# Performance work log

Measured on AMD Instinct MI355X. Metric: run time of the kernel, lower is better.

Reference implementation:

```python
import jax, jax.numpy as jnp
import numpy as np

C = 256; COUT = 256; G = 8; GC = C // G; K = 3; P = K * K
PAD = 1; DIL = 1; STR = 1
EPS = 1e-5


def _group_norm(x, gamma, beta, groups=32, eps=EPS):
    # x: (N,H,W,C), torch.nn.GroupNorm semantics (biased var)
    N, H, W, Cc = x.shape
    xg = x.reshape(N, H, W, groups, Cc // groups)
    mu = xg.mean(axis=(1, 2, 4), keepdims=True)
    var = xg.var(axis=(1, 2, 4), keepdims=True)
    xg = (xg - mu) * jax.lax.rsqrt(var + eps)
    return xg.reshape(N, H, W, Cc) * gamma + beta


def _conv2d(x, w, b, stride=1, pad=1, groups=1):
    y = jax.lax.conv_general_dilated(
        x, w, (stride, stride), [(pad, pad), (pad, pad)],
        dimension_numbers=('NHWC', 'HWIO', 'NHWC'),
        feature_group_count=groups)
    return y + b


def _bilinear_gather(img, px, py, Hin, Win):
    x0 = jnp.floor(px); y0 = jnp.floor(py)
    wx1 = px - x0; wy1 = py - y0
    out = jnp.zeros(img.shape[:1] + px.shape[1:] + img.shape[-1:], img.dtype)
    for xi, wx in ((x0, 1.0 - wx1), (x0 + 1.0, wx1)):
        for yi, wy in ((y0, 1.0 - wy1), (y0 + 1.0, wy1)):
            valid = (xi >= 0) & (xi < Win) & (yi >= 0) & (yi < Hin)
            idx = (jnp.clip(yi, 0, Hin - 1) * Win + jnp.clip(xi, 0, Win - 1)).astype(jnp.int32)
            vals = jnp.take_along_axis(img, idx[..., None], axis=1)
            out = out + vals * (wx * wy * valid)[..., None]
    return out


def _forward(x, w_in, b_in, dw_w, dw_b, ln_g, ln_b, w_off, b_off, w_mask, b_mask,
             w_out, b_out, gn1_g, gn1_b, conv1_w, conv1_b, gn2_g, gn2_b,
             down_w, down_b, gn3_g, gn3_b):
    xs = jnp.transpose(x, (0, 2, 3, 1))  # NHWC
    N, H, W, _ = xs.shape
    # ---- DCNv3 ----
    x_proj = xs @ w_in + b_in                              # input_proj
    t = _conv2d(xs, dw_w, dw_b, stride=STR, pad=(K - 1) // 2, groups=C)  # depthwise
    mu = t.mean(-1, keepdims=True)
    var = t.var(-1, keepdims=True)
    t = (t - mu) * jax.lax.rsqrt(var + EPS) * ln_g + ln_b  # LayerNorm
    t = jax.nn.gelu(t, approximate=False)
    offset = (t @ w_off + b_off).reshape(N, H, W, G, P, 2)  # (x,y) pairs
    mask = jax.nn.softmax((t @ w_mask + b_mask).reshape(N, H, W, G, P), axis=-1)

    Hin, Win = H + 2 * PAD, W + 2 * PAD
    xp = jnp.pad(x_proj, ((0, 0), (PAD, PAD), (PAD, PAD), (0, 0)))
    base = (DIL * (K - 1)) // 2 + 0.5
    ref_y = (base + jnp.arange(H, dtype=xs.dtype) * STR) / Hin
    ref_x = (base + jnp.arange(W, dtype=xs.dtype) * STR) / Win
    ry, rx = jnp.meshgrid(ref_y, ref_x, indexing='ij')
    ref = jnp.stack([rx, ry], -1)[None, :, :, None, None, :]  # (1,H,W,1,1,2)
    d = jnp.arange(K, dtype=xs.dtype) * DIL - (DIL * (K - 1)) // 2
    gx, gy = jnp.meshgrid(d, d, indexing='ij')  # x varies fastest over axis0 (torch order)
    grid = jnp.stack([gx / Win, gy / Hin], -1).reshape(P, 2)
    spatial = jnp.array([Win, Hin], xs.dtype)
    loc = ref + grid + offset / spatial          # normalized [0,1], offset_scale=1
    px = loc[..., 0] * Win - 0.5                 # align_corners=False pixel coords
    py = loc[..., 1] * Hin - 0.5

    L = H * W
    img = xp.reshape(N, Hin * Win, G, GC).transpose(0, 2, 1, 3).reshape(N * G, Hin * Win, GC)
    pxf = jnp.transpose(px, (0, 3, 1, 2, 4)).reshape(N * G, L * P)
    pyf = jnp.transpose(py, (0, 3, 1, 2, 4)).reshape(N * G, L * P)
    sampled = _bilinear_gather(img, pxf, pyf, Hin, Win).reshape(N, G, L, P, GC)
    m = jnp.transpose(mask, (0, 3, 1, 2, 4)).reshape(N, G, L, P)
    agg = jnp.einsum('nglpc,nglp->nglc', sampled, m)
    y = agg.transpose(0, 2, 1, 3).reshape(N, H, W, C)
    y = y @ w_out + b_out                        # output_proj
    # ---- block_out ----
    y = jax.nn.silu(_group_norm(y, gn1_g, gn1_b))
    y = _conv2d(y, conv1_w, conv1_b, stride=1, pad=1)
    y = jax.nn.silu(_group_norm(y, gn2_g, gn2_b))
    # ---- down_sample ----
    y = _conv2d(y, down_w, down_b, stride=2, pad=1)
    y = _group_norm(y, gn3_g, gn3_b)
    return jnp.transpose(y, (0, 3, 1, 2))  # back to NCHW


def setup_inputs() -> dict:
    key = jax.random.key(0)
    ks = jax.random.split(key, 10)
    f = jnp.float32
    nrm = lambda k, shape, s: jax.random.normal(k, shape, dtype=f) * s
    N, H, W = 4, 64, 64
    return {
        'x': jax.random.normal(ks[0], (N, C, H, W), dtype=f),
        'w_in': nrm(ks[1], (C, C), 0.05), 'b_in': jnp.zeros((C,), f),
        'dw_w': nrm(ks[2], (K, K, 1, C), 0.1), 'dw_b': jnp.zeros((C,), f),
        'ln_g': jnp.ones((C,), f), 'ln_b': jnp.zeros((C,), f),
        'w_off': nrm(ks[3], (C, 2 * G * P), 0.02), 'b_off': nrm(ks[4], (2 * G * P,), 1.0),
        'w_mask': nrm(ks[5], (C, G * P), 0.02), 'b_mask': jnp.zeros((G * P,), f),
        'w_out': nrm(ks[6], (C, C), 0.05), 'b_out': jnp.zeros((C,), f),
        'gn1_g': jnp.ones((C,), f), 'gn1_b': jnp.zeros((C,), f),
        'conv1_w': nrm(ks[7], (3, 3, C, C), 0.02), 'conv1_b': jnp.zeros((C,), f),
        'gn2_g': jnp.ones((C,), f), 'gn2_b': jnp.zeros((C,), f),
        'down_w': nrm(ks[8], (3, 3, C, COUT), 0.02), 'down_b': jnp.zeros((COUT,), f),
        'gn3_g': jnp.ones((COUT,), f), 'gn3_b': jnp.zeros((COUT,), f),
    }


def reference(x, w_in, b_in, dw_w, dw_b, ln_g, ln_b, w_off, b_off, w_mask, b_mask,
              w_out, b_out, gn1_g, gn1_b, conv1_w, conv1_b, gn2_g, gn2_b,
              down_w, down_b, gn3_g, gn3_b):
    return _forward(x, w_in, b_in, dw_w, dw_b, ln_g, ln_b, w_off, b_off, w_mask,
                    b_mask, w_out, b_out, gn1_g, gn1_b, conv1_w, conv1_b,
                    gn2_g, gn2_b, down_w, down_b, gn3_g, gn3_b)
```

## Files before the change

kernel.cpp:

```cpp
#include <hip/hip_runtime.h>
#include <hip/hip_bf16.h>
#include <math.h>


typedef __attribute__((ext_vector_type(8))) short bf16x8;
typedef __attribute__((ext_vector_type(4))) float f32x4;

__device__ __forceinline__ float blo(unsigned u){
  union { unsigned int i; float f; } v; v.i = u<<16; return v.f;
}
__device__ __forceinline__ float bhi(unsigned u){
  union { unsigned int i; float f; } v; v.i = u & 0xffff0000u; return v.f;
}
__device__ __forceinline__ unsigned short f2b(float f){
  __hip_bfloat16 h = __float2bfloat16(f);
  return *reinterpret_cast<unsigned short*>(&h);
}
__device__ __forceinline__ unsigned pk2(float lo, float hi){
  return (unsigned)f2b(lo) | ((unsigned)f2b(hi)<<16);
}

__device__ __forceinline__ void gload16(const void* g, void* l){
  auto gp = reinterpret_cast<const __attribute__((address_space(1))) uint32_t*>(
      reinterpret_cast<uintptr_t>(g));
  auto lp = reinterpret_cast<__attribute__((address_space(3))) uint32_t*>(
      reinterpret_cast<uintptr_t>(l));
  __builtin_amdgcn_global_load_lds(gp, lp, 16, 0, 0);
}

__global__ __launch_bounds__(256) void k_prep(
    const float* __restrict__ x,
    const float* __restrict__ w_in, const float* __restrict__ w_out,
    const float* __restrict__ conv1_w, const float* __restrict__ down_w,
    const float* __restrict__ w_off, const float* __restrict__ w_mask,
    const float* __restrict__ b_off, const float* __restrict__ b_mask,
    __hip_bfloat16* __restrict__ w_inT, __hip_bfloat16* __restrict__ w_outT,
    __hip_bfloat16* __restrict__ c1T, __hip_bfloat16* __restrict__ dnT,
    __hip_bfloat16* __restrict__ w_omT, float* __restrict__ bias_om,
    float* __restrict__ stats, __hip_bfloat16* __restrict__ R3,
    __hip_bfloat16* __restrict__ xs)
{
  int b = blockIdx.x;
  if (b < 160){
    __shared__ float tl[32][257];
    const float* W; __hip_bfloat16* WT; int Kd, kb;
    if (b < 8)      { W = w_in;    WT = w_inT;  Kd = 256;  kb = b; }
    else if (b <16) { W = w_out;   WT = w_outT; Kd = 256;  kb = b-8; }
    else if (b <88) { W = conv1_w; WT = c1T;    Kd = 2304; kb = b-16; }
    else            { W = down_w;  WT = dnT;    Kd = 2304; kb = b-88; }
    int k0 = kb*32;
    #pragma unroll
    for (int dk=0; dk<32; dk++) tl[dk][threadIdx.x] = W[(size_t)(k0+dk)*256 + threadIdx.x];
    __syncthreads();
    #pragma unroll
    for (int r=0; r<32; r++){
      int co = r*8 + (threadIdx.x>>5);
      int dk = threadIdx.x&31;
      WT[(size_t)co*Kd + k0 + dk] = __float2bfloat16(tl[dk][co]);
    }
  } else if (b < 416){
    int n = b - 160, k = threadIdx.x;
    float v = (n<144) ? w_off[(size_t)k*144 + n] : (n<216 ? w_mask[(size_t)k*72 + (n-144)] : 0.f);
    w_omT[(size_t)n*256 + k] = __float2bfloat16(v);
    if (k==0) bias_om[n] = (n<144) ? b_off[n] : (n<216 ? b_mask[n-144] : 0.f);
  } else if (b < 546){
    int gid = (b-416)*8 + (threadIdx.x>>5);
    if (gid >= 1040) return;
    int n = gid/260; int ci = gid - n*260;
    int r, c;
    if (ci < 66){ r = 0; c = ci; }
    else if (ci < 132){ r = 65; c = ci-66; }
    else { int q = ci-132; r = 1 + (q>>1); c = (q&1) ? 65 : 0; }
    uint4* p = (uint4*)(R3 + ((size_t)((n*66+r)*66+c))*256) + (threadIdx.x&31);
    *p = make_uint4(0,0,0,0);
  } else if (b == 546){
    stats[threadIdx.x] = 0.f;
    stats[256+threadIdx.x] = 0.f;
    stats[512+threadIdx.x] = 0.f;
  } else {
    __shared__ float tile[32][33];
    int t = b - 547;
    int n = t >> 10;
    int c0 = ((t >> 7) & 7) * 32;
    int hw0 = (t & 127) * 32;
    int tx = threadIdx.x & 31, ty = threadIdx.x >> 5;
    #pragma unroll
    for (int ii=0; ii<4; ii++){
      int ci = ty + ii*8;
      tile[ci][tx] = x[(size_t)(n*256 + c0+ci)*4096 + hw0 + tx];
    }
    __syncthreads();
    #pragma unroll
    for (int ii=0; ii<4; ii++){
      int hwi = ty + ii*8;
      xs[((size_t)n*4096 + hw0+hwi)*256 + c0 + tx] = __float2bfloat16(tile[tx][hwi]);
    }
  }
}

template<int AMODE, int OMODE, int STRIDE, int KTOT, int NSHIFT>
__global__ __launch_bounds__(256) void k_mm(
    const __hip_bfloat16* __restrict__ A, const __hip_bfloat16* __restrict__ Bt,
    const float* __restrict__ bias, float* __restrict__ OF, __hip_bfloat16* __restrict__ OH,
    float* __restrict__ stats)
{
  constexpr int AROWS = 64;
  constexpr int MI = AROWS/32;
  constexpr int WROWS = AROWS/2;
  constexpr int JA = AROWS*128/4096;
  constexpr int BUFSZ = AROWS*128 + 16384;
  __shared__ uint4 lds4[3*BUFSZ/16];
  char* ldsc = (char*)lds4;
  const int tid = threadIdx.x;
  const int lane = tid & 63;
  const int wv = tid >> 6;
  const int wr = wv >> 1, wc = wv & 1;

  int id = blockIdx.y * gridDim.x + blockIdx.x;
  int cpx = (gridDim.x * gridDim.y) >> 3;
  int sw = (id & 7) * cpx + (id >> 3);
  const int m0 = (sw >> 1) * AROWS, n0 = (sw & 1) * 128;

  const int swz_s = ((tid >> 3) & 7) << 4;
  const int cby = ((tid & 7) << 4) ^ swz_s;
  const int kl = cby >> 1;
  int aoff[JA], boff[4];
  #pragma unroll
  for (int j=0;j<JA;j++){
    int row = j*32 + (tid>>3);
    if (AMODE==0){
      aoff[j] = (m0 + row) * KTOT + kl;
    } else {
      int m = m0 + row;
      int n, ho, wo;
      if (STRIDE==1){ n = m>>12; ho = (m>>6)&63; wo = m&63; }
      else          { n = m>>10; ho = (m>>5)&31; wo = m&31; }
      aoff[j] = ((n*66 + ho*STRIDE)*66 + wo*STRIDE)*256 + kl;
    }
  }
  #pragma unroll
  for (int j=0;j<4;j++) boff[j] = (n0 + j*32 + (tid>>3)) * KTOT + kl;
  char* ldsst = ldsc + wv*1024;

  const int fr = lane & 15;
  const int kb = (lane >> 4) << 4;
  const int swz_r = (fr & 7) << 4;
  int aRow[MI], bRow[4];
  #pragma unroll
  for (int i=0;i<MI;i++) aRow[i] = (wr*WROWS + i*16 + fr) * 128;
  #pragma unroll
  for (int i=0;i<4;i++)  bRow[i] = AROWS*128 + (wc*64 + i*16 + fr) * 128;
  int cb[2];
  cb[0] = kb ^ swz_r;
  cb[1] = (64 | kb) ^ swz_r;

  float bn[4];
  #pragma unroll
  for (int ni=0;ni<4;ni++) bn[ni] = bias[n0 + wc*64 + ni*16 + fr];

  f32x4 acc[MI][4];
  #pragma unroll
  for (int mi=0;mi<MI;mi++)
    #pragma unroll
    for (int ni=0;ni<4;ni++)
      acc[mi][ni] = (f32x4){0.f,0.f,0.f,0.f};

  auto STAGE = [&](int buf, int t){
    const int k0 = t*64;
    int astep;
    if (AMODE==1){
      int tap = k0 >> 8;
      int kh = (tap>=6) ? 2 : (tap>=3 ? 1 : 0);
      int kw = tap - kh*3;
      astep = (kh*66 + kw)*256 + (k0 & 255);
    } else astep = k0;
    char* db = ldsst + buf*BUFSZ;
    #pragma unroll
    for (int j=0;j<JA;j++) gload16(A + aoff[j] + astep, db + j*4096);
    #pragma unroll
    for (int j=0;j<4;j++)  gload16(Bt + boff[j] + k0, db + AROWS*128 + j*4096);
  };

  constexpr int NT = KTOT / 64;
  STAGE(0, 0);
  STAGE(1, 1);
  asm volatile("s_waitcnt vmcnt(6)" ::: "memory");
  __builtin_amdgcn_s_barrier();
  __builtin_amdgcn_sched_barrier(0);
  for (int t=0; t<NT; ++t){
    if (t+2 < NT) STAGE((t+2)%3, t+2);
    char* cbase = ldsc + (t%3)*BUFSZ;
    __builtin_amdgcn_s_setprio(1);
    #pragma unroll
    for (int kk=0; kk<2; kk++){
      bf16x8 av[MI], bv[4];
      #pragma unroll
      for (int i=0;i<MI;i++) av[i] = *(const bf16x8*)(cbase + aRow[i] + cb[kk]);
      #pragma unroll
      for (int i=0;i<4;i++)  bv[i] = *(const bf16x8*)(cbase + bRow[i] + cb[kk]);
      #pragma unroll
      for (int mi=0;mi<MI;mi++)
        #pragma unroll
        for (int ni=0;ni<4;ni++)
          acc[mi][ni] = __builtin_amdgcn_mfma_f32_16x16x32_bf16(av[mi], bv[ni], acc[mi][ni], 0,0,0);
    }
    __builtin_amdgcn_s_setprio(0);
    if (t < NT-1){
      if (t+2 < NT) asm volatile("s_waitcnt vmcnt(6)" ::: "memory");
      else          asm volatile("s_waitcnt vmcnt(0)" ::: "memory");
      __builtin_amdgcn_s_barrier();
      __builtin_amdgcn_sched_barrier(0);
    }
  }

  float sni[4] = {0.f,0.f,0.f,0.f};
  float qni[4] = {0.f,0.f,0.f,0.f};
  #pragma unroll
  for (int mi=0;mi<MI;mi++){
    #pragma unroll
    for (int r=0;r<4;r++){
      int gr = m0 + wr*WROWS + mi*16 + (lane>>4)*4 + r;
      #pragma unroll
      for (int ni=0;ni<4;ni++){
        int gc = n0 + wc*64 + ni*16 + fr;
        float v = acc[mi][ni][r] + bn[ni];
        if (NSHIFT){ sni[ni] += v; qni[ni] += v*v; }
        if (OMODE==0){
          OH[(size_t)gr*256 + gc] = __float2bfloat16(v);
        } else if (OMODE==1){
          int n = gr>>12, h = (gr>>6)&63, w = gr&63;
          OH[((size_t)((n*66)+(h+1))*66 + (w+1))*256 + gc] = __float2bfloat16(v);
        } else {
          if (gc < 216) OF[(size_t)gr*216 + gc] = v;
        }
      }
    }
  }
  if (NSHIFT){
    #pragma unroll
    for (int ni=0;ni<4;ni++){
      #pragma unroll
      for (int msk=16; msk<64; msk<<=1){
        sni[ni] += __shfl_xor(sni[ni], msk);
        qni[ni] += __shfl_xor(qni[ni], msk);
      }
      #pragma unroll
      for (int msk=1; msk<8; msk<<=1){
        sni[ni] += __shfl_xor(sni[ni], msk);
        qni[ni] += __shfl_xor(qni[ni], msk);
      }
    }
    __syncthreads();
    float* ls = (float*)ldsc;
    if (tid < 32) ls[tid] = 0.f;
    __syncthreads();
    if ((lane & 7) == 0 && (lane & 48) == 0){
      int oct = (lane>>3) & 1;
      #pragma unroll
      for (int ni=0;ni<4;ni++){
        int idx = wc*8 + ni*2 + oct;
        atomicAdd(&ls[idx], sni[ni]);
        atomicAdd(&ls[16+idx], qni[ni]);
      }
    }
    __syncthreads();
    if (tid < 16){
      int gg = (m0>>NSHIFT)*32 + (n0>>3) + tid;
      atomicAdd(&stats[gg*2+0], ls[tid]);
      atomicAdd(&stats[gg*2+1], ls[16+tid]);
    }
  }
}

__global__ __launch_bounds__(256) void k_dwln(
    const __hip_bfloat16* __restrict__ xs, const float* __restrict__ dw_w, const float* __restrict__ dw_b,
    const float* __restrict__ ln_g, const float* __restrict__ ln_b, __hip_bfloat16* __restrict__ t)
{
  __shared__ float lw[9*256];
  __shared__ float lb[256], lg[256], lbt[256];
  int tid = threadIdx.x;
  #pragma unroll
  for (int p=0;p<9;p++) lw[p*256+tid] = dw_w[p*256+tid];
  lb[tid] = dw_b[tid]; lg[tid] = ln_g[tid]; lbt[tid] = ln_b[tid];
  __syncthreads();
  int posl = tid>>5, cg = tid&31, c0 = cg*8;
  int pos = blockIdx.x*8 + posl;
  int nb = pos>>12, h = (pos>>6)&63, w = pos&63;
  float v[8];
  #pragma unroll
  for (int k=0;k<8;k++) v[k] = lb[c0+k];
  #pragma unroll
  for (int kh=0;kh<3;kh++){
    int hin = h+kh-1;
    if (hin<0||hin>=64) continue;
    #pragma unroll
    for (int kw=0;kw<3;kw++){
      int win = w+kw-1;
      if (win<0||win>=64) continue;
      const unsigned short* xr = (const unsigned short*)xs + ((size_t)((nb*64+hin)*64+win))*256 + c0;
      uint4 u = *(const uint4*)xr;
      const float* wr = &lw[(kh*3+kw)*256 + c0];
      v[0] += blo(u.x)*wr[0]; v[1] += bhi(u.x)*wr[1];
      v[2] += blo(u.y)*wr[2]; v[3] += bhi(u.y)*wr[3];
      v[4] += blo(u.z)*wr[4]; v[5] += bhi(u.z)*wr[5];
      v[6] += blo(u.w)*wr[6]; v[7] += bhi(u.w)*wr[7];
    }
  }
  float s=0.f, s2=0.f;
  #pragma unroll
  for (int k=0;k<8;k++){ s += v[k]; s2 += v[k]*v[k]; }
  #pragma unroll
  for (int m=1;m<32;m<<=1){ s += __shfl_xor(s,m); s2 += __shfl_xor(s2,m); }
  float mu = s*(1.f/256.f);
  float var = s2*(1.f/256.f) - mu*mu;
  float rstd = rsqrtf(var + 1e-5f);
  float ge[8];
  #pragma unroll
  for (int k=0;k<8;k++){
    float xn = (v[k]-mu)*rstd*lg[c0+k] + lbt[c0+k];
    ge[k] = 0.5f*xn*(1.f + erff(xn*0.70710678118654752f));
  }
  uint4 o;
  o.x = pk2(ge[0],ge[1]); o.y = pk2(ge[2],ge[3]);
  o.z = pk2(ge[4],ge[5]); o.w = pk2(ge[6],ge[7]);
  *(uint4*)((unsigned short*)t + (size_t)pos*256 + c0) = o;
}

__global__ __launch_bounds__(256) void k_sample(
    const __hip_bfloat16* __restrict__ xp, const float* __restrict__ D, __hip_bfloat16* __restrict__ y)
{
  int tid = threadIdx.x;
  int pp = tid>>5;
  int g = (tid>>2)&7, li = tid&3;
  int pos = blockIdx.x*8 + pp;
  int nb = pos >> 12, h = (pos >> 6) & 63, w = pos & 63;
  const float* Dp = D + (size_t)pos*216;
  const float* offp = Dp + g*18;
  const float* mskp = Dp + 144 + g*9;
  float mr[9];
  #pragma unroll
  for (int p=0;p<9;p++) mr[p] = mskp[p];
  float mx = mr[0];
  #pragma unroll
  for (int p=1;p<9;p++) mx = fmaxf(mx, mr[p]);
  float ssum = 0.f;
  #pragma unroll
  for (int p=0;p<9;p++){ mr[p] = __expf(mr[p]-mx); ssum += mr[p]; }
  float rinv = 1.f/ssum;
  const unsigned short* img = (const unsigned short*)xp + (size_t)nb*4356*256 + g*32 + li*8;
  float a0=0,a1=0,a2=0,a3=0,a4=0,a5=0,a6=0,a7=0;
  #pragma unroll
  for (int p=0;p<9;p++){
    int di = p/3 - 1, dj = p%3 - 1;
    float2 off = *(const float2*)(offp + p*2);
    float px = (float)(w + 1 + di) + off.x;
    float py = (float)(h + 1 + dj) + off.y;
    float x0f = floorf(px), y0f = floorf(py);
    float wx1 = px - x0f, wy1 = py - y0f;
    float wx0 = 1.f - wx1, wy0 = 1.f - wy1;
    int x0 = (int)x0f, y0 = (int)y0f;
    float s0=0,s1=0,s2=0,s3=0,s4=0,s5=0,s6=0,s7=0;
    #pragma unroll
    for (int cy=0;cy<2;cy++){
      int yi = y0+cy;
      if (yi<0||yi>=66) continue;
      float wy = cy ? wy1 : wy0;
      #pragma unroll
      for (int cx=0;cx<2;cx++){
        int xi = x0+cx;
        if (xi<0||xi>=66) continue;
        float wq = (cx ? wx1 : wx0)*wy;
        uint4 u = *(const uint4*)(img + (size_t)(yi*66+xi)*256);
        s0 += blo(u.x)*wq; s1 += bhi(u.x)*wq;
        s2 += blo(u.y)*wq; s3 += bhi(u.y)*wq;
        s4 += blo(u.z)*wq; s5 += bhi(u.z)*wq;
        s6 += blo(u.w)*wq; s7 += bhi(u.w)*wq;
      }
    }
    float mp = mr[p]*rinv;
    a0 += s0*mp; a1 += s1*mp; a2 += s2*mp; a3 += s3*mp;
    a4 += s4*mp; a5 += s5*mp; a6 += s6*mp; a7 += s7*mp;
  }
  uint4 o;
  o.x = pk2(a0,a1); o.y = pk2(a2,a3); o.z = pk2(a4,a5); o.w = pk2(a6,a7);
  *(uint4*)((unsigned short*)y + (size_t)pos*256 + g*32 + li*8) = o;
}

__global__ __launch_bounds__(256) void k_gnapply(
    const __hip_bfloat16* __restrict__ X, const float* __restrict__ stats,
    const float* __restrict__ gamma, const float* __restrict__ beta,
    __hip_bfloat16* __restrict__ OH, int nmain)
{
  int b = blockIdx.x;
  int tid = threadIdx.x;
  if (b >= nmain){
    int gid = (b - nmain)*8 + (tid>>5);
    if (gid >= 1040) return;
    int n = gid/260; int ci = gid - n*260;
    int r, c;
    if (ci < 66){ r = 0; c = ci; }
    else if (ci < 132){ r = 65; c = ci-66; }
    else { int q = ci-132; r = 1 + (q>>1); c = (q&1) ? 65 : 0; }
    uint4* p = (uint4*)(OH + ((size_t)((n*66+r)*66+c))*256) + (tid&31);
    *p = make_uint4(0,0,0,0);
    return;
  }
  int row = b*8 + (tid>>5);
  int grp = tid & 31;
  int c0 = grp*8;
  int nb = row >> 12;
  float S  = stats[(nb*32+grp)*2+0];
  float S2 = stats[(nb*32+grp)*2+1];
  const float inv = 1.f/32768.f;
  float mu = S*inv;
  float rs = rsqrtf(S2*inv - mu*mu + 1e-5f);
  float4 g0 = *(const float4*)(gamma + c0), g1 = *(const float4*)(gamma + c0 + 4);
  float4 bt0 = *(const float4*)(beta + c0), bt1 = *(const float4*)(beta + c0 + 4);
  uint4 u = *(const uint4*)((const unsigned short*)X + (size_t)row*256 + c0);
  float v[8] = { blo(u.x), bhi(u.x), blo(u.y), bhi(u.y), blo(u.z), bhi(u.z), blo(u.w), bhi(u.w) };
  float gm[8] = { g0.x,g0.y,g0.z,g0.w,g1.x,g1.y,g1.z,g1.w };
  float bb[8] = { bt0.x,bt0.y,bt0.z,bt0.w,bt1.x,bt1.y,bt1.z,bt1.w };
  #pragma unroll
  for (int k=0;k<8;k++){
    float t = (v[k]-mu)*rs*gm[k] + bb[k];
    v[k] = t / (1.f + expf(-t));
  }
  int h = (row>>6)&63, w = row&63;
  uint4 o;
  o.x = pk2(v[0],v[1]); o.y = pk2(v[2],v[3]); o.z = pk2(v[4],v[5]); o.w = pk2(v[6],v[7]);
  *(uint4*)((unsigned short*)OH + ((size_t)((nb*66)+(h+1))*66 + (w+1))*256 + c0) = o;
}

__global__ __launch_bounds__(256) void k_gnout(
    const __hip_bfloat16* __restrict__ X, const float* __restrict__ stats,
    const float* __restrict__ gamma, const float* __restrict__ beta, float* __restrict__ out)
{
  __shared__ float val[8][1024];
  int nb = blockIdx.x >> 5, cg = blockIdx.x & 31;
  int c0 = cg*8;
  float S  = stats[(nb*32+cg)*2+0];
  float S2 = stats[(nb*32+cg)*2+1];
  const float inv = 1.f/8192.f;
  float mu = S*inv;
  float rs = rsqrtf(S2*inv - mu*mu + 1e-5f);
  float4 g0 = *(const float4*)(gamma + c0), g1 = *(const float4*)(gamma + c0 + 4);
  float4 bt0 = *(const float4*)(beta + c0), bt1 = *(const float4*)(beta + c0 + 4);
  float gm[8] = { g0.x,g0.y,g0.z,g0.w,g1.x,g1.y,g1.z,g1.w };
  float bb[8] = { bt0.x,bt0.y,bt0.z,bt0.w,bt1.x,bt1.y,bt1.z,bt1.w };
  #pragma unroll
  for (int k=0;k<4;k++){
    int pos = k*256 + threadIdx.x;
    uint4 u = *(const uint4*)((const unsigned short*)X + ((size_t)(nb*1024+pos))*256 + c0);
    float v[8] = { blo(u.x), bhi(u.x), blo(u.y), bhi(u.y), blo(u.z), bhi(u.z), blo(u.w), bhi(u.w) };
    #pragma unroll
    for (int q=0;q<8;q++) val[q][pos] = (v[q]-mu)*rs*gm[q] + bb[q];
  }
  __syncthreads();
  int ch = threadIdx.x>>5, pl = threadIdx.x&31;
  float* orow = out + (((size_t)(nb*256 + c0 + ch))<<10);
  #pragma unroll
  for (int j=0;j<32;j++) orow[pl + j*32] = val[ch][pl + j*32];
}

extern "C" void kernel_launch(void* const* d_in, const int* in_sizes, int n_in,
                              void* d_out, int out_size, void* d_ws, size_t ws_size,
                              hipStream_t stream) {
  const float* x      = (const float*)d_in[0];
  const float* w_in   = (const float*)d_in[1];
  const float* b_in   = (const float*)d_in[2];
  const float* dw_w   = (const float*)d_in[3];
  const float* dw_b   = (const float*)d_in[4];
  const float* ln_g   = (const float*)d_in[5];
  const float* ln_b   = (const float*)d_in[6];
  const float* w_off  = (const float*)d_in[7];
  const float* b_off  = (const float*)d_in[8];
  const float* w_mask = (const float*)d_in[9];
  const float* b_mask = (const float*)d_in[10];
  const float* w_out  = (const float*)d_in[11];
  const float* b_out  = (const float*)d_in[12];
  const float* gn1_g  = (const float*)d_in[13];
  const float* gn1_b  = (const float*)d_in[14];
  const float* conv1_w= (const float*)d_in[15];
  const float* conv1_b= (const float*)d_in[16];
  const float* gn2_g  = (const float*)d_in[17];
  const float* gn2_b  = (const float*)d_in[18];
  const float* down_w = (const float*)d_in[19];
  const float* down_b = (const float*)d_in[20];
  const float* gn3_g  = (const float*)d_in[21];
  const float* gn3_b  = (const float*)d_in[22];
  float* out = (float*)d_out;

  char* wsb = (char*)d_ws;
  __hip_bfloat16* R0h = (__hip_bfloat16*)wsb;
  float* R1f = (float*)(wsb + 16777216);
  __hip_bfloat16* R1h = (__hip_bfloat16*)(wsb + 16777216);
  __hip_bfloat16* R2 = (__hip_bfloat16*)(wsb + 33554432);
  __hip_bfloat16* R3 = (__hip_bfloat16*)(wsb + 41943040);
  __hip_bfloat16* R4 = (__hip_bfloat16*)(wsb + 50864128);
  char* R5 = wsb + 59785216;
  __hip_bfloat16* w_inT  = (__hip_bfloat16*)R5;
  __hip_bfloat16* w_outT = (__hip_bfloat16*)(R5 + 131072);
  __hip_bfloat16* w_omT  = (__hip_bfloat16*)(R5 + 262144);
  __hip_bfloat16* c1T    = (__hip_bfloat16*)(R5 + 393216);
  __hip_bfloat16* dnT    = (__hip_bfloat16*)(R5 + 1572864);
  float* bias_om         = (float*)(R5 + 2752512);
  float* stats           = (float*)(R5 + 2753536);

  k_prep<<<4643, 256, 0, stream>>>(x, w_in, w_out, conv1_w, down_w, w_off, w_mask, b_off, b_mask,
                                   w_inT, w_outT, c1T, dnT, w_omT, bias_om, stats, R3, R2);
  k_mm<0,1,1,256,0><<<dim3(256,2), 256, 0, stream>>>(R2, w_inT, b_in, nullptr, R3, nullptr);
  k_dwln<<<2048, 256, 0, stream>>>(R2, dw_w, dw_b, ln_g, ln_b, R4);
  k_mm<0,2,1,256,0><<<dim3(256,2), 256, 0, stream>>>(R4, w_omT, bias_om, R1f, nullptr, nullptr);
  k_sample<<<2048, 256, 0, stream>>>(R3, R1f, R2);
  k_mm<0,0,1,256,12><<<dim3(256,2), 256, 0, stream>>>(R2, w_outT, b_out, nullptr, R0h, stats);
  k_gnapply<<<2048+130, 256, 0, stream>>>(R0h, stats, gn1_g, gn1_b, R4, 2048);
  k_mm<1,0,1,2304,12><<<dim3(256,2), 256, 0, stream>>>(R4, c1T, conv1_b, nullptr, R1h, stats+256);
  k_gnapply<<<2048+130, 256, 0, stream>>>(R1h, stats+256, gn2_g, gn2_b, R3, 2048);
  k_mm<1,0,2,2304,10><<<dim3(64,2), 256, 0, stream>>>(R3, dnT, down_b, nullptr, R0h, stats+512);
  k_gnout<<<128, 256, 0, stream>>>(R0h, stats+512, gn3_g, gn3_b, out);
}
```

Before: 235.3 us.

## Fuse all stages into one persistent kernel with atomic grid barriers

Replaces the eleven separate launches with a single persistent kernel of 512 blocks that runs every stage in turn, separated by atomic-counter grid barriers. Elementwise stages are remapped so each block processes rows it produced in the preceding GEMM tile, and the final strided conv switches to 32-row tiles over 256 blocks. The goal is to remove launch gaps and tail effects between kernels and to improve cache locality. In exchange the kernel depends on all 512 blocks being co-resident (two per CU), spends time in spin barriers, and leaves blocks idle during the smaller stages.

```diff
diff --git a/kernel.cpp b/kernel.cpp
--- a/kernel.cpp
+++ b/kernel.cpp
@@ -3,6 +3,8 @@
 #include <math.h>
 
 
+#define NBLK 512
+
 typedef __attribute__((ext_vector_type(8))) short bf16x8;
 typedef __attribute__((ext_vector_type(4))) float f32x4;
 
@@ -21,14 +23,26 @@
 }
 
 __device__ __forceinline__ void gload16(const void* g, void* l){
-  auto gp = reinterpret_cast<const __attribute__((address_space(1))) uint32_t*>(
+  auto gp = reinterpret_cast<const __attribute__((address_space(1))) unsigned*>(
       reinterpret_cast<uintptr_t>(g));
-  auto lp = reinterpret_cast<__attribute__((address_space(3))) uint32_t*>(
+  auto lp = reinterpret_cast<__attribute__((address_space(3))) unsigned*>(
       reinterpret_cast<uintptr_t>(l));
   __builtin_amdgcn_global_load_lds(gp, lp, 16, 0, 0);
 }
 
-__global__ __launch_bounds__(256) void k_prep(
+__device__ __forceinline__ void gridsync(unsigned* c){
+  __syncthreads();
+  if (threadIdx.x == 0){
+    __threadfence();
+    atomicAdd(c, 1u);
+    while (__hip_atomic_load(c, __ATOMIC_RELAXED, __HIP_MEMORY_SCOPE_AGENT) < (unsigned)NBLK)
+      __builtin_amdgcn_s_sleep(1);
+    __threadfence();
+  }
+  __syncthreads();
+}
+
+__device__ void prep_unit(int b, char* smem,
     const float* __restrict__ x,
     const float* __restrict__ w_in, const float* __restrict__ w_out,
     const float* __restrict__ conv1_w, const float* __restrict__ down_w,
@@ -40,9 +54,9 @@
     float* __restrict__ stats, __hip_bfloat16* __restrict__ R3,
     __hip_bfloat16* __restrict__ xs)
 {
-  int b = blockIdx.x;
+  __syncthreads();
   if (b < 160){
-    __shared__ float tl[32][257];
+    float (*tl)[257] = (float(*)[257])smem;
     const float* W; __hip_bfloat16* WT; int Kd, kb;
     if (b < 8)      { W = w_in;    WT = w_inT;  Kd = 256;  kb = b; }
     else if (b <16) { W = w_out;   WT = w_outT; Kd = 256;  kb = b-8; }
@@ -78,7 +92,7 @@
     stats[256+threadIdx.x] = 0.f;
     stats[512+threadIdx.x] = 0.f;
   } else {
-    __shared__ float tile[32][33];
+    float (*tile)[33] = (float(*)[33])smem;
     int t = b - 547;
     int n = t >> 10;
     int c0 = ((t >> 7) & 7) * 32;
@@ -98,27 +112,25 @@
   }
 }
 
-template<int AMODE, int OMODE, int STRIDE, int KTOT, int NSHIFT>
-__global__ __launch_bounds__(256) void k_mm(
+#define WAITV(n) asm volatile("s_waitcnt vmcnt(" #n ")" ::: "memory")
+
+template<int AMODE, int OMODE, int STRIDE, int KTOT, int NSHIFT, int AROWS, int NWG>
+__device__ void mm_body(int id,
     const __hip_bfloat16* __restrict__ A, const __hip_bfloat16* __restrict__ Bt,
     const float* __restrict__ bias, float* __restrict__ OF, __hip_bfloat16* __restrict__ OH,
-    float* __restrict__ stats)
+    float* __restrict__ stats, char* ldsc)
 {
-  constexpr int AROWS = 64;
   constexpr int MI = AROWS/32;
   constexpr int WROWS = AROWS/2;
-  constexpr int JA = AROWS*128/4096;
+  constexpr int JA = AROWS/32;
+  constexpr int SL = JA + 4;
   constexpr int BUFSZ = AROWS*128 + 16384;
-  __shared__ uint4 lds4[3*BUFSZ/16];
-  char* ldsc = (char*)lds4;
   const int tid = threadIdx.x;
   const int lane = tid & 63;
   const int wv = tid >> 6;
   const int wr = wv >> 1, wc = wv & 1;
 
-  int id = blockIdx.y * gridDim.x + blockIdx.x;
-  int cpx = (gridDim.x * gridDim.y) >> 3;
-  int sw = (id & 7) * cpx + (id >> 3);
+  int sw = (id & 7) * (NWG >> 3) + (id >> 3);
   const int m0 = (sw >> 1) * AROWS, n0 = (sw & 1) * 128;
 
   const int swz_s = ((tid >> 3) & 7) << 4;
@@ -184,7 +196,7 @@
   constexpr int NT = KTOT / 64;
   STAGE(0, 0);
   STAGE(1, 1);
-  asm volatile("s_waitcnt vmcnt(6)" ::: "memory");
+  if constexpr (SL==6) WAITV(6); else WAITV(5);
   __builtin_amdgcn_s_barrier();
   __builtin_amdgcn_sched_barrier(0);
   for (int t=0; t<NT; ++t){
@@ -206,8 +218,8 @@
     }
     __builtin_amdgcn_s_setprio(0);
     if (t < NT-1){
-      if (t+2 < NT) asm volatile("s_waitcnt vmcnt(6)" ::: "memory");
-      else          asm volatile("s_waitcnt vmcnt(0)" ::: "memory");
+      if (t+2 < NT){ if constexpr (SL==6) WAITV(6); else WAITV(5); }
+      else WAITV(0);
       __builtin_amdgcn_s_barrier();
       __builtin_amdgcn_sched_barrier(0);
     }
@@ -272,19 +284,13 @@
   }
 }
 
-__global__ __launch_bounds__(256) void k_dwln(
-    const __hip_bfloat16* __restrict__ xs, const float* __restrict__ dw_w, const float* __restrict__ dw_b,
-    const float* __restrict__ ln_g, const float* __restrict__ ln_b, __hip_bfloat16* __restrict__ t)
+__device__ void dwln_unit(int l, const __hip_bfloat16* __restrict__ xs,
+    const float* lw, const float* lb, const float* lg, const float* lbt,
+    __hip_bfloat16* __restrict__ t)
 {
-  __shared__ float lw[9*256];
-  __shared__ float lb[256], lg[256], lbt[256];
   int tid = threadIdx.x;
-  #pragma unroll
-  for (int p=0;p<9;p++) lw[p*256+tid] = dw_w[p*256+tid];
-  lb[tid] = dw_b[tid]; lg[tid] = ln_g[tid]; lbt[tid] = ln_b[tid];
-  __syncthreads();
   int posl = tid>>5, cg = tid&31, c0 = cg*8;
-  int pos = blockIdx.x*8 + posl;
+  int pos = l*8 + posl;
   int nb = pos>>12, h = (pos>>6)&63, w = pos&63;
   float v[8];
   #pragma unroll
@@ -326,17 +332,16 @@
   *(uint4*)((unsigned short*)t + (size_t)pos*256 + c0) = o;
 }
 
-__global__ __launch_bounds__(256) void k_sample(
-    const __hip_bfloat16* __restrict__ xp, const float* __restrict__ D, __hip_bfloat16* __restrict__ y)
+__device__ void sample_unit(int l, const float* Ds,
+    const __hip_bfloat16* __restrict__ xp, __hip_bfloat16* __restrict__ y)
 {
   int tid = threadIdx.x;
   int pp = tid>>5;
   int g = (tid>>2)&7, li = tid&3;
-  int pos = blockIdx.x*8 + pp;
+  int pos = l*8 + pp;
   int nb = pos >> 12, h = (pos >> 6) & 63, w = pos & 63;
-  const float* Dp = D + (size_t)pos*216;
-  const float* offp = Dp + g*18;
-  const float* mskp = Dp + 144 + g*9;
+  const float* offp = Ds + pp*216 + g*18;
+  const float* mskp = Ds + pp*216 + 144 + g*9;
   float mr[9];
   #pragma unroll
   for (int p=0;p<9;p++) mr[p] = mskp[p];
@@ -352,9 +357,9 @@
   #pragma unroll
   for (int p=0;p<9;p++){
     int di = p/3 - 1, dj = p%3 - 1;
-    float2 off = *(const float2*)(offp + p*2);
-    float px = (float)(w + 1 + di) + off.x;
-    float py = (float)(h + 1 + dj) + off.y;
+    float ox = offp[p*2], oy = offp[p*2+1];
+    float px = (float)(w + 1 + di) + ox;
+    float py = (float)(h + 1 + dj) + oy;
     float x0f = floorf(px), y0f = floorf(py);
     float wx1 = px - x0f, wy1 = py - y0f;
     float wx0 = 1.f - wx1, wy0 = 1.f - wy1;
@@ -386,26 +391,12 @@
   *(uint4*)((unsigned short*)y + (size_t)pos*256 + g*32 + li*8) = o;
 }
 
-__global__ __launch_bounds__(256) void k_gnapply(
-    const __hip_bfloat16* __restrict__ X, const float* __restrict__ stats,
-    const float* __restrict__ gamma, const float* __restrict__ beta,
-    __hip_bfloat16* __restrict__ OH, int nmain)
+__device__ void gnap_main(int u, const __hip_bfloat16* __restrict__ X,
+    const float* __restrict__ stats, const float* __restrict__ gamma,
+    const float* __restrict__ beta, __hip_bfloat16* __restrict__ OH)
 {
-  int b = blockIdx.x;
   int tid = threadIdx.x;
-  if (b >= nmain){
-    int gid = (b - nmain)*8 + (tid>>5);
-    if (gid >= 1040) return;
-    int n = gid/260; int ci = gid - n*260;
-    int r, c;
-    if (ci < 66){ r = 0; c = ci; }
-    else if (ci < 132){ r = 65; c = ci-66; }
-    else { int q = ci-132; r = 1 + (q>>1); c = (q&1) ? 65 : 0; }
-    uint4* p = (uint4*)(OH + ((size_t)((n*66+r)*66+c))*256) + (tid&31);
-    *p = make_uint4(0,0,0,0);
-    return;
-  }
-  int row = b*8 + (tid>>5);
+  int row = u*8 + (tid>>5);
   int grp = tid & 31;
   int c0 = grp*8;
   int nb = row >> 12;
@@ -416,8 +407,8 @@
   float rs = rsqrtf(S2*inv - mu*mu + 1e-5f);
   float4 g0 = *(const float4*)(gamma + c0), g1 = *(const float4*)(gamma + c0 + 4);
   float4 bt0 = *(const float4*)(beta + c0), bt1 = *(const float4*)(beta + c0 + 4);
-  uint4 u = *(const uint4*)((const unsigned short*)X + (size_t)row*256 + c0);
-  float v[8] = { blo(u.x), bhi(u.x), blo(u.y), bhi(u.y), blo(u.z), bhi(u.z), blo(u.w), bhi(u.w) };
+  uint4 u4 = *(const uint4*)((const unsigned short*)X + (size_t)row*256 + c0);
+  float v[8] = { blo(u4.x), bhi(u4.x), blo(u4.y), bhi(u4.y), blo(u4.z), bhi(u4.z), blo(u4.w), bhi(u4.w) };
   float gm[8] = { g0.x,g0.y,g0.z,g0.w,g1.x,g1.y,g1.z,g1.w };
   float bb[8] = { bt0.x,bt0.y,bt0.z,bt0.w,bt1.x,bt1.y,bt1.z,bt1.w };
   #pragma unroll
@@ -431,12 +422,24 @@
   *(uint4*)((unsigned short*)OH + ((size_t)((nb*66)+(h+1))*66 + (w+1))*256 + c0) = o;
 }
 
-__global__ __launch_bounds__(256) void k_gnout(
-    const __hip_bfloat16* __restrict__ X, const float* __restrict__ stats,
-    const float* __restrict__ gamma, const float* __restrict__ beta, float* __restrict__ out)
+__device__ void gnap_border(int u, __hip_bfloat16* __restrict__ OH){
+  int gid = u*8 + (threadIdx.x>>5);
+  if (gid >= 1040) return;
+  int n = gid/260; int ci = gid - n*260;
+  int r, c;
+  if (ci < 66){ r = 0; c = ci; }
+  else if (ci < 132){ r = 65; c = ci-66; }
+  else { int q = ci-132; r = 1 + (q>>1); c = (q&1) ? 65 : 0; }
+  uint4* p = (uint4*)(OH + ((size_t)((n*66+r)*66+c))*256) + (threadIdx.x&31);
+  *p = make_uint4(0,0,0,0);
+}
+
+__device__ void gnout_unit(int u, const __hip_bfloat16* __restrict__ X,
+    const float* __restrict__ stats, const float* __restrict__ gamma,
+    const float* __restrict__ beta, float* __restrict__ out, char* smem)
 {
-  __shared__ float val[8][1024];
-  int nb = blockIdx.x >> 5, cg = blockIdx.x & 31;
+  float (*val)[1024] = (float(*)[1024])smem;
+  int nb = u >> 5, cg = u & 31;
   int c0 = cg*8;
   float S  = stats[(nb*32+cg)*2+0];
   float S2 = stats[(nb*32+cg)*2+1];
@@ -450,8 +453,8 @@
   #pragma unroll
   for (int k=0;k<4;k++){
     int pos = k*256 + threadIdx.x;
-    uint4 u = *(const uint4*)((const unsigned short*)X + ((size_t)(nb*1024+pos))*256 + c0);
-    float v[8] = { blo(u.x), bhi(u.x), blo(u.y), bhi(u.y), blo(u.z), bhi(u.z), blo(u.w), bhi(u.w) };
+    uint4 u4 = *(const uint4*)((const unsigned short*)X + ((size_t)(nb*1024+pos))*256 + c0);
+    float v[8] = { blo(u4.x), bhi(u4.x), blo(u4.y), bhi(u4.y), blo(u4.z), bhi(u4.z), blo(u4.w), bhi(u4.w) };
     #pragma unroll
     for (int q=0;q<8;q++) val[q][pos] = (v[q]-mu)*rs*gm[q] + bb[q];
   }
@@ -460,6 +463,102 @@
   float* orow = out + (((size_t)(nb*256 + c0 + ch))<<10);
   #pragma unroll
   for (int j=0;j<32;j++) orow[pl + j*32] = val[ch][pl + j*32];
+}
+
+__global__ __launch_bounds__(256, 2) void k_mega(
+    const float* __restrict__ x,
+    const float* __restrict__ w_in, const float* __restrict__ b_in,
+    const float* __restrict__ dw_w, const float* __restrict__ dw_b,
+    const float* __restrict__ ln_g, const float* __restrict__ ln_b,
+    const float* __restrict__ w_off, const float* __restrict__ b_off,
+    const float* __restrict__ w_mask, const float* __restrict__ b_mask,
+    const float* __restrict__ w_out, const float* __restrict__ b_out,
+    const float* __restrict__ gn1_g, const float* __restrict__ gn1_b,
+    const float* __restrict__ conv1_w, const float* __restrict__ conv1_b,
+    const float* __restrict__ gn2_g, const float* __restrict__ gn2_b,
+    const float* __restrict__ down_w, const float* __restrict__ down_b,
+    const float* __restrict__ gn3_g, const float* __restrict__ gn3_b,
+    float* __restrict__ out,
+    __hip_bfloat16* R0h, float* R1f, __hip_bfloat16* R2,
+    __hip_bfloat16* R3, __hip_bfloat16* R4,
+    __hip_bfloat16* w_inT, __hip_bfloat16* w_outT, __hip_bfloat16* w_omT,
+    __hip_bfloat16* c1T, __hip_bfloat16* dnT,
+    float* bias_om, float* stats, unsigned* sync)
+{
+  __shared__ __align__(16) char SMEM[73728];
+  __hip_bfloat16* R1h = (__hip_bfloat16*)R1f;
+  const int bid = blockIdx.x;
+  const int s8 = bid>>3, x8 = bid&7;
+
+  for (int b = bid; b < 4643; b += NBLK)
+    prep_unit(b, SMEM, x, w_in, w_out, conv1_w, down_w, w_off, w_mask, b_off, b_mask,
+              w_inT, w_outT, c1T, dnT, w_omT, bias_om, stats, R3, R2);
+  gridsync(sync+0);
+
+  mm_body<0,1,1,256,0,64,NBLK>(bid, R2, w_inT, b_in, nullptr, R3, nullptr, SMEM);
+  __syncthreads();
+  {
+    float* lw = (float*)SMEM;
+    float* lb = (float*)(SMEM+9216);
+    float* lg = (float*)(SMEM+10240);
+    float* lbt= (float*)(SMEM+11264);
+    int tid = threadIdx.x;
+    #pragma unroll
+    for (int p=0;p<9;p++) lw[p*256+tid] = dw_w[p*256+tid];
+    lb[tid] = dw_b[tid]; lg[tid] = ln_g[tid]; lbt[tid] = ln_b[tid];
+    __syncthreads();
+    #pragma unroll
+    for (int j=0;j<4;j++){
+      int l = (x8>>1)*512 + (s8*2+(x8&1))*4 + j;
+      dwln_unit(l, R2, lw, lb, lg, lbt, R4);
+    }
+  }
+  gridsync(sync+1);
+
+  mm_body<0,2,1,256,0,64,NBLK>(bid, R4, w_omT, bias_om, R1f, nullptr, nullptr, SMEM);
+  gridsync(sync+2);
+
+  #pragma unroll
+  for (int j=0;j<4;j++){
+    int l = (x8>>1)*512 + (s8*2+(x8&1))*4 + j;
+    __syncthreads();
+    float4* dst = (float4*)SMEM;
+    const float4* src = (const float4*)(R1f + (size_t)l*8*216);
+    int tid = threadIdx.x;
+    if (tid < 216){ dst[tid] = src[tid]; dst[tid+216] = src[tid+216]; }
+    __syncthreads();
+    sample_unit(l, (const float*)SMEM, R3, R2);
+  }
+  gridsync(sync+3);
+
+  mm_body<0,0,1,256,12,64,NBLK>(bid, R2, w_outT, b_out, nullptr, R0h, stats, SMEM);
+  gridsync(sync+4);
+
+  #pragma unroll
+  for (int j=0;j<4;j++){
+    int u = (x8>>1)*512 + (s8*2+(x8&1))*4 + j;
+    gnap_main(u, R0h, stats, gn1_g, gn1_b, R4);
+  }
+  for (int u = bid; u < 130; u += NBLK) gnap_border(u, R4);
+  gridsync(sync+5);
+
+  mm_body<1,0,1,2304,12,64,NBLK>(bid, R4, c1T, conv1_b, nullptr, R1h, stats+256, SMEM);
+  gridsync(sync+6);
+
+  #pragma unroll
+  for (int j=0;j<4;j++){
+    int u = (x8>>1)*512 + (s8*2+(x8&1))*4 + j;
+    gnap_main(u, R1h, stats+256, gn2_g, gn2_b, R3);
+  }
+  for (int u = bid; u < 130; u += NBLK) gnap_border(u, R3);
+  gridsync(sync+7);
+
+  if (bid < 256)
+    mm_body<1,0,2,2304,10,32,256>(bid, R3, dnT, down_b, nullptr, R0h, stats+512, SMEM);
+  gridsync(sync+8);
+
+  if (bid < 128)
+    gnout_unit(bid, R0h, stats+512, gn3_g, gn3_b, out, SMEM);
 }
 
 extern "C" void kernel_launch(void* const* d_in, const int* in_sizes, int n_in,
@@ -493,7 +592,6 @@
   char* wsb = (char*)d_ws;
   __hip_bfloat16* R0h = (__hip_bfloat16*)wsb;
   float* R1f = (float*)(wsb + 16777216);
-  __hip_bfloat16* R1h = (__hip_bfloat16*)(wsb + 16777216);
   __hip_bfloat16* R2 = (__hip_bfloat16*)(wsb + 33554432);
   __hip_bfloat16* R3 = (__hip_bfloat16*)(wsb + 41943040);
   __hip_bfloat16* R4 = (__hip_bfloat16*)(wsb + 50864128);
@@ -505,17 +603,13 @@
   __hip_bfloat16* dnT    = (__hip_bfloat16*)(R5 + 1572864);
   float* bias_om         = (float*)(R5 + 2752512);
   float* stats           = (float*)(R5 + 2753536);
-
-  k_prep<<<4643, 256, 0, stream>>>(x, w_in, w_out, conv1_w, down_w, w_off, w_mask, b_off, b_mask,
-                                   w_inT, w_outT, c1T, dnT, w_omT, bias_om, stats, R3, R2);
-  k_mm<0,1,1,256,0><<<dim3(256,2), 256, 0, stream>>>(R2, w_inT, b_in, nullptr, R3, nullptr);
-  k_dwln<<<2048, 256, 0, stream>>>(R2, dw_w, dw_b, ln_g, ln_b, R4);
-  k_mm<0,2,1,256,0><<<dim3(256,2), 256, 0, stream>>>(R4, w_omT, bias_om, R1f, nullptr, nullptr);
-  k_sample<<<2048, 256, 0, stream>>>(R3, R1f, R2);
-  k_mm<0,0,1,256,12><<<dim3(256,2), 256, 0, stream>>>(R2, w_outT, b_out, nullptr, R0h, stats);
-  k_gnapply<<<2048+130, 256, 0, stream>>>(R0h, stats, gn1_g, gn1_b, R4, 2048);
-  k_mm<1,0,1,2304,12><<<dim3(256,2), 256, 0, stream>>>(R4, c1T, conv1_b, nullptr, R1h, stats+256);
-  k_gnapply<<<2048+130, 256, 0, stream>>>(R1h, stats+256, gn2_g, gn2_b, R3, 2048);
-  k_mm<1,0,2,2304,10><<<dim3(64,2), 256, 0, stream>>>(R3, dnT, down_b, nullptr, R0h, stats+512);
-  k_gnout<<<128, 256, 0, stream>>>(R0h, stats+512, gn3_g, gn3_b, out);
-}
+  unsigned* syncc        = (unsigned*)(R5 + 2756608);
+
+  hipMemsetAsync(syncc, 0, 64, stream);
+  k_mega<<<NBLK, 256, 0, stream>>>(
+      x, w_in, b_in, dw_w, dw_b, ln_g, ln_b, w_off, b_off, w_mask, b_mask,
+      w_out, b_out, gn1_g, gn1_b, conv1_w, conv1_b, gn2_g, gn2_b,
+      down_w, down_b, gn3_g, gn3_b, out,
+      R0h, R1f, R2, R3, R4, w_inT, w_outT, w_omT, c1T, dnT,
+      bias_om, stats, syncc);
+}
```

New measurement: 672.9 us. 186% more time.

## Merge input-projection GEMM and depthwise-LN into one launch; stage sampler params in LDS

Applied to the files above, without the earlier changes.

The input_proj GEMM and the depthwise conv + LayerNorm + GELU kernel both read only xs, so they now run as one launch: the first 512 blocks do the GEMM and the remaining 2048 do the depthwise work. This removes a launch boundary and lets the two independent jobs overlap on the GPU. The sampler kernel now copies each block's offset/mask rows from global memory into shared memory with coalesced float4 loads before use. The price is that the dwln blocks now reserve the GEMM's full 72KB of LDS, which may cut their occupancy.

```diff
diff --git a/kernel.cpp b/kernel.cpp
--- a/kernel.cpp
+++ b/kernel.cpp
@@ -21,12 +21,14 @@
 }
 
 __device__ __forceinline__ void gload16(const void* g, void* l){
-  auto gp = reinterpret_cast<const __attribute__((address_space(1))) uint32_t*>(
+  auto gp = reinterpret_cast<const __attribute__((address_space(1))) unsigned*>(
       reinterpret_cast<uintptr_t>(g));
-  auto lp = reinterpret_cast<__attribute__((address_space(3))) uint32_t*>(
+  auto lp = reinterpret_cast<__attribute__((address_space(3))) unsigned*>(
       reinterpret_cast<uintptr_t>(l));
   __builtin_amdgcn_global_load_lds(gp, lp, 16, 0, 0);
 }
+
+#define WAITV(n) asm volatile("s_waitcnt vmcnt(" #n ")" ::: "memory")
 
 __global__ __launch_bounds__(256) void k_prep(
     const float* __restrict__ x,
@@ -98,27 +100,23 @@
   }
 }
 
-template<int AMODE, int OMODE, int STRIDE, int KTOT, int NSHIFT>
-__global__ __launch_bounds__(256) void k_mm(
+template<int AMODE, int OMODE, int STRIDE, int KTOT, int NSHIFT, int NWG>
+__device__ __forceinline__ void mm_body(int id,
     const __hip_bfloat16* __restrict__ A, const __hip_bfloat16* __restrict__ Bt,
     const float* __restrict__ bias, float* __restrict__ OF, __hip_bfloat16* __restrict__ OH,
-    float* __restrict__ stats)
+    float* __restrict__ stats, char* ldsc)
 {
   constexpr int AROWS = 64;
-  constexpr int MI = AROWS/32;
-  constexpr int WROWS = AROWS/2;
-  constexpr int JA = AROWS*128/4096;
+  constexpr int MI = 2;
+  constexpr int WROWS = 32;
+  constexpr int JA = 2;
   constexpr int BUFSZ = AROWS*128 + 16384;
-  __shared__ uint4 lds4[3*BUFSZ/16];
-  char* ldsc = (char*)lds4;
   const int tid = threadIdx.x;
   const int lane = tid & 63;
   const int wv = tid >> 6;
   const int wr = wv >> 1, wc = wv & 1;
 
-  int id = blockIdx.y * gridDim.x + blockIdx.x;
-  int cpx = (gridDim.x * gridDim.y) >> 3;
-  int sw = (id & 7) * cpx + (id >> 3);
+  int sw = (id & 7) * (NWG >> 3) + (id >> 3);
   const int m0 = (sw >> 1) * AROWS, n0 = (sw & 1) * 128;
 
   const int swz_s = ((tid >> 3) & 7) << 4;
@@ -184,7 +182,7 @@
   constexpr int NT = KTOT / 64;
   STAGE(0, 0);
   STAGE(1, 1);
-  asm volatile("s_waitcnt vmcnt(6)" ::: "memory");
+  WAITV(6);
   __builtin_amdgcn_s_barrier();
   __builtin_amdgcn_sched_barrier(0);
   for (int t=0; t<NT; ++t){
@@ -206,8 +204,8 @@
     }
     __builtin_amdgcn_s_setprio(0);
     if (t < NT-1){
-      if (t+2 < NT) asm volatile("s_waitcnt vmcnt(6)" ::: "memory");
-      else          asm volatile("s_waitcnt vmcnt(0)" ::: "memory");
+      if (t+2 < NT){ WAITV(6); }
+      else WAITV(0);
       __builtin_amdgcn_s_barrier();
       __builtin_amdgcn_sched_barrier(0);
     }
@@ -272,19 +270,24 @@
   }
 }
 
-__global__ __launch_bounds__(256) void k_dwln(
-    const __hip_bfloat16* __restrict__ xs, const float* __restrict__ dw_w, const float* __restrict__ dw_b,
-    const float* __restrict__ ln_g, const float* __restrict__ ln_b, __hip_bfloat16* __restrict__ t)
-{
-  __shared__ float lw[9*256];
-  __shared__ float lb[256], lg[256], lbt[256];
+template<int AMODE, int OMODE, int STRIDE, int KTOT, int NSHIFT, int NWG>
+__global__ __launch_bounds__(256) void k_mm(
+    const __hip_bfloat16* __restrict__ A, const __hip_bfloat16* __restrict__ Bt,
+    const float* __restrict__ bias, float* __restrict__ OF, __hip_bfloat16* __restrict__ OH,
+    float* __restrict__ stats)
+{
+  __shared__ __align__(16) char SMEM[73728];
+  int id = blockIdx.y * gridDim.x + blockIdx.x;
+  mm_body<AMODE,OMODE,STRIDE,KTOT,NSHIFT,NWG>(id, A, Bt, bias, OF, OH, stats, SMEM);
+}
+
+__device__ __forceinline__ void dwln_unit(int l, const __hip_bfloat16* __restrict__ xs,
+    const float* lw, const float* lb, const float* lg, const float* lbt,
+    __hip_bfloat16* __restrict__ t)
+{
   int tid = threadIdx.x;
-  #pragma unroll
-  for (int p=0;p<9;p++) lw[p*256+tid] = dw_w[p*256+tid];
-  lb[tid] = dw_b[tid]; lg[tid] = ln_g[tid]; lbt[tid] = ln_b[tid];
-  __syncthreads();
   int posl = tid>>5, cg = tid&31, c0 = cg*8;
-  int pos = blockIdx.x*8 + posl;
+  int pos = l*8 + posl;
   int nb = pos>>12, h = (pos>>6)&63, w = pos&63;
   float v[8];
   #pragma unroll
@@ -326,17 +329,48 @@
   *(uint4*)((unsigned short*)t + (size_t)pos*256 + c0) = o;
 }
 
+__global__ __launch_bounds__(256) void k_p1(
+    const __hip_bfloat16* __restrict__ xs, const __hip_bfloat16* __restrict__ w_inT,
+    const float* __restrict__ b_in, __hip_bfloat16* __restrict__ R3,
+    const float* __restrict__ dw_w, const float* __restrict__ dw_b,
+    const float* __restrict__ ln_g, const float* __restrict__ ln_b,
+    __hip_bfloat16* __restrict__ t)
+{
+  __shared__ __align__(16) char SMEM[73728];
+  int bid = blockIdx.x;
+  if (bid < 512){
+    mm_body<0,1,1,256,0,512>(bid, xs, w_inT, b_in, nullptr, R3, nullptr, SMEM);
+  } else {
+    float* lw = (float*)SMEM;
+    float* lb = (float*)(SMEM+9216);
+    float* lg = (float*)(SMEM+10240);
+    float* lbt= (float*)(SMEM+11264);
+    int tid = threadIdx.x;
+    #pragma unroll
+    for (int p=0;p<9;p++) lw[p*256+tid] = dw_w[p*256+tid];
+    lb[tid] = dw_b[tid]; lg[tid] = ln_g[tid]; lbt[tid] = ln_b[tid];
+    __syncthreads();
+    dwln_unit(bid-512, xs, lw, lb, lg, lbt, t);
+  }
+}
+
 __global__ __launch_bounds__(256) void k_sample(
     const __hip_bfloat16* __restrict__ xp, const float* __restrict__ D, __hip_bfloat16* __restrict__ y)
 {
+  __shared__ float Ds[1728];
   int tid = threadIdx.x;
+  {
+    float4* dst = (float4*)Ds;
+    const float4* src = (const float4*)(D + (size_t)blockIdx.x*1728);
+    if (tid < 216){ dst[tid] = src[tid]; dst[tid+216] = src[tid+216]; }
+    __syncthreads();
+  }
   int pp = tid>>5;
   int g = (tid>>2)&7, li = tid&3;
   int pos = blockIdx.x*8 + pp;
   int nb = pos >> 12, h = (pos >> 6) & 63, w = pos & 63;
-  const float* Dp = D + (size_t)pos*216;
-  const float* offp = Dp + g*18;
-  const float* mskp = Dp + 144 + g*9;
+  const float* offp = Ds + pp*216 + g*18;
+  const float* mskp = Ds + pp*216 + 144 + g*9;
   float mr[9];
   #pragma unroll
   for (int p=0;p<9;p++) mr[p] = mskp[p];
@@ -352,9 +386,9 @@
   #pragma unroll
   for (int p=0;p<9;p++){
     int di = p/3 - 1, dj = p%3 - 1;
-    float2 off = *(const float2*)(offp + p*2);
-    float px = (float)(w + 1 + di) + off.x;
-    float py = (float)(h + 1 + dj) + off.y;
+    float ox = offp[p*2], oy = offp[p*2+1];
+    float px = (float)(w + 1 + di) + ox;
+    float py = (float)(h + 1 + dj) + oy;
     float x0f = floorf(px), y0f = floorf(py);
     float wx1 = px - x0f, wy1 = py - y0f;
     float wx0 = 1.f - wx1, wy0 = 1.f - wy1;
@@ -508,14 +542,13 @@
 
   k_prep<<<4643, 256, 0, stream>>>(x, w_in, w_out, conv1_w, down_w, w_off, w_mask, b_off, b_mask,
                                    w_inT, w_outT, c1T, dnT, w_omT, bias_om, stats, R3, R2);
-  k_mm<0,1,1,256,0><<<dim3(256,2), 256, 0, stream>>>(R2, w_inT, b_in, nullptr, R3, nullptr);
-  k_dwln<<<2048, 256, 0, stream>>>(R2, dw_w, dw_b, ln_g, ln_b, R4);
-  k_mm<0,2,1,256,0><<<dim3(256,2), 256, 0, stream>>>(R4, w_omT, bias_om, R1f, nullptr, nullptr);
+  k_p1<<<2560, 256, 0, stream>>>(R2, w_inT, b_in, R3, dw_w, dw_b, ln_g, ln_b, R4);
+  k_mm<0,2,1,256,0,512><<<dim3(256,2), 256, 0, stream>>>(R4, w_omT, bias_om, R1f, nullptr, nullptr);
   k_sample<<<2048, 256, 0, stream>>>(R3, R1f, R2);
-  k_mm<0,0,1,256,12><<<dim3(256,2), 256, 0, stream>>>(R2, w_outT, b_out, nullptr, R0h, stats);
+  k_mm<0,0,1,256,12,512><<<dim3(256,2), 256, 0, stream>>>(R2, w_outT, b_out, nullptr, R0h, stats);
   k_gnapply<<<2048+130, 256, 0, stream>>>(R0h, stats, gn1_g, gn1_b, R4, 2048);
-  k_mm<1,0,1,2304,12><<<dim3(256,2), 256, 0, stream>>>(R4, c1T, conv1_b, nullptr, R1h, stats+256);
+  k_mm<1,0,1,2304,12,512><<<dim3(256,2), 256, 0, stream>>>(R4, c1T, conv1_b, nullptr, R1h, stats+256);
   k_gnapply<<<2048+130, 256, 0, stream>>>(R1h, stats+256, gn2_g, gn2_b, R3, 2048);
-  k_mm<1,0,2,2304,10><<<dim3(64,2), 256, 0, stream>>>(R3, dnT, down_b, nullptr, R0h, stats+512);
+  k_mm<1,0,2,2304,10,128><<<dim3(64,2), 256, 0, stream>>>(R3, dnT, down_b, nullptr, R0h, stats+512);
   k_gnout<<<128, 256, 0, stream>>>(R0h, stats+512, gn3_g, gn3_b, out);
 }
```

New measurement: 244.5 us. 1.04x slower.
